# Kernel tuning notes

Hardware: AMD Instinct MI355X
Metric: run time of the kernel (lower is better)

## Reference

```python
import jax, jax.numpy as jnp
import numpy as np

N = 4096      # nodes
HID = 512     # hidden_size
HEADS = 8
DH = HID // HEADS
EPS = 1e-5    # BatchNorm eps


def setup_inputs() -> dict:
    key = jax.random.key(0)
    ks = jax.random.split(key, 16)
    h = jax.random.normal(ks[0], (N, HID), jnp.float32)
    # sparse adjacency (~degree 32) with self-loops so every row has a neighbor
    A = (jax.random.uniform(ks[1], (N, N)) < 0.008).astype(jnp.float32)
    A = jnp.maximum(A, jnp.eye(N, dtype=jnp.float32))
    w = lambda k, shp: jax.random.normal(k, shp, jnp.float32) * 0.02
    return {
        "A": A, "h": h,
        "Wq": w(ks[2], (HID, HID)), "bq": jnp.zeros((HID,), jnp.float32),
        "Wk": w(ks[3], (HID, HID)), "bk": jnp.zeros((HID,), jnp.float32),
        "Wv": w(ks[4], (HID, HID)), "bv": jnp.zeros((HID,), jnp.float32),
        "Wo": w(ks[5], (HID, HID)), "bo": jnp.zeros((HID,), jnp.float32),
        "bn1_g": jnp.ones((HID,), jnp.float32), "bn1_b": jnp.zeros((HID,), jnp.float32),
        "bn2_g": jnp.ones((HID,), jnp.float32), "bn2_b": jnp.zeros((HID,), jnp.float32),
        "W1": w(ks[6], (HID, 2 * HID)), "b1": jnp.zeros((2 * HID,), jnp.float32),
        "W2": w(ks[7], (2 * HID, HID)), "b2": jnp.zeros((HID,), jnp.float32),
    }


def _batchnorm(x, g, b):
    # BatchNorm1d training mode: stats over the node (batch) axis
    m = jnp.mean(x, axis=0)
    v = jnp.var(x, axis=0)
    return g * (x - m) * jax.lax.rsqrt(v + EPS) + b


def _layer(A, h, Wq, bq, Wk, bk, Wv, bv, Wo, bo,
           bn1_g, bn1_b, bn2_g, bn2_b, W1, b1, W2, b2):
    n = h.shape[0]
    q = (h @ Wq + bq).reshape(n, HEADS, DH)
    k = (h @ Wk + bk).reshape(n, HEADS, DH)
    v = (h @ Wv + bv).reshape(n, HEADS, DH)
    # scores [heads, n, m], masked by adjacency
    scores = jnp.einsum('nhd,mhd->hnm', q, k) / np.float32(np.sqrt(DH))
    scores = jnp.where(A[None, :, :] > 0, scores, jnp.float32(-1e9))
    attn = jax.nn.softmax(scores, axis=-1)
    o = jnp.einsum('hnm,mhd->nhd', attn, v).reshape(n, HID)
    h1 = o @ Wo + bo
    h = _batchnorm(h + h1, bn1_g, bn1_b)
    h2 = jax.nn.relu(h @ W1 + b1) @ W2 + b2
    return _batchnorm(h + h2, bn2_g, bn2_b)


def reference(A, h, Wq, bq, Wk, bk, Wv, bv, Wo, bo,
              bn1_g, bn1_b, bn2_g, bn2_b, W1, b1, W2, b2):
    return _layer(A, h, Wq, bq, Wk, bk, Wv, bv, Wo, bo,
                  bn1_g, bn1_b, bn2_g, bn2_b, W1, b1, W2, b2)
```

## Files before the change

kernel.cpp:

```cpp
#include <hip/hip_runtime.h>

#define N_NODES 4096
#define HID 512
#define HEADS 8
#define DH 64
#define EPS 1e-5f
#define MAXD 128

typedef __attribute__((ext_vector_type(8))) short bf16x8;
typedef __attribute__((ext_vector_type(4))) float f32x4;

__device__ __forceinline__ unsigned short f2bf(float f) {
    unsigned int u = __float_as_uint(f);
    unsigned int r = (u + 0x7FFFu + ((u >> 16) & 1u)) >> 16;
    return (unsigned short)r;
}
__device__ __forceinline__ float blo(unsigned int u) {
    return __uint_as_float(u << 16);
}
__device__ __forceinline__ float bhi(unsigned int u) {
    return __uint_as_float(u & 0xffff0000u);
}

__device__ __forceinline__ void gld_lds16(const void* g, void* l) {
    __builtin_amdgcn_global_load_lds(
        (const __attribute__((address_space(1))) unsigned int*)g,
        (__attribute__((address_space(3))) unsigned int*)l, 16, 0, 0);
}

template<int BN, int EPI>
__global__ __launch_bounds__(256) void gemm_bf16(
    const unsigned short* __restrict__ Xb, const unsigned short* __restrict__ Wt,
    const float* __restrict__ bias, const float* __restrict__ res,
    float* __restrict__ outf, unsigned short* __restrict__ outb,
    float* __restrict__ sum, float* __restrict__ sumsq,
    int K, int Nc)
{
    constexpr int WM = (BN == 128) ? 4 : 2;
    __shared__ __align__(16) unsigned short As[128 * 64];
    __shared__ __align__(16) unsigned short Bs[BN * 64];

    const int tid = threadIdx.x;
    const int lane = tid & 63;
    const int wv = tid >> 6;
    const int wm = (BN == 128) ? (wv >> 1) : wv;
    const int wn = (BN == 128) ? (wv & 1) : 0;
    const int m0 = blockIdx.y * 128, n0 = blockIdx.x * BN;
    const int lc = lane & 15, lq = lane >> 4;

    const int srow = tid >> 3;
    const int schunk = (tid & 7) ^ (srow & 7);
    unsigned short* ldsA = As + tid * 8;
    unsigned short* ldsB = Bs + tid * 8;

    const int rs0 = lq ^ (lc & 7);
    const int rs1 = (4 + lq) ^ (lc & 7);

    f32x4 acc[WM][4] = {};

    for (int k0 = 0; k0 < K; k0 += 64) {
        const unsigned short* gA = Xb + (size_t)(m0 + srow) * K + k0 + schunk * 8;
        const unsigned short* gB = Wt + (size_t)(n0 + srow) * K + k0 + schunk * 8;
        #pragma unroll
        for (int p = 0; p < 4; ++p)
            gld_lds16(gA + (size_t)(p * 32) * K, ldsA + p * 2048);
        #pragma unroll
        for (int p = 0; p < BN / 32; ++p)
            gld_lds16(gB + (size_t)(p * 32) * K, ldsB + p * 2048);
        __syncthreads();

        #pragma unroll
        for (int h = 0; h < 2; ++h) {
            const int rs = h ? rs1 : rs0;
            bf16x8 af[WM], bfr[4];
            #pragma unroll
            for (int i = 0; i < WM; ++i)
                af[i] = *(const bf16x8*)&As[(wm * (WM * 16) + i * 16 + lc) * 64 + rs * 8];
            #pragma unroll
            for (int j = 0; j < 4; ++j)
                bfr[j] = *(const bf16x8*)&Bs[(wn * 64 + j * 16 + lc) * 64 + rs * 8];
            #pragma unroll
            for (int i = 0; i < WM; ++i)
                #pragma unroll
                for (int j = 0; j < 4; ++j)
                    acc[i][j] = __builtin_amdgcn_mfma_f32_16x16x32_bf16(af[i], bfr[j], acc[i][j], 0, 0, 0);
        }
        __syncthreads();
    }

    float cs[4] = {}, css[4] = {};
    #pragma unroll
    for (int i = 0; i < WM; ++i) {
        #pragma unroll
        for (int j = 0; j < 4; ++j) {
            const int gr0 = m0 + wm * (WM * 16) + i * 16 + lq * 4;
            const int gc = n0 + wn * 64 + j * 16 + lc;
            const float bi = bias[gc];
            #pragma unroll
            for (int r = 0; r < 4; ++r) {
                float val = acc[i][j][r] + bi;
                size_t off = (size_t)(gr0 + r) * Nc + gc;
                if (EPI == 0)      outb[off] = f2bf(val);
                else if (EPI == 1) outb[off] = f2bf(fmaxf(val, 0.f));
                else {
                    val += res[off];
                    outf[off] = val;
                    cs[j] += val; css[j] += val * val;
                }
            }
        }
    }
    if (EPI == 2) {
        #pragma unroll
        for (int j = 0; j < 4; ++j) {
            float s = cs[j], ss = css[j];
            s += __shfl_xor(s, 16); s += __shfl_xor(s, 32);
            ss += __shfl_xor(ss, 16); ss += __shfl_xor(ss, 32);
            if (lq == 0) {
                const int gc = n0 + wn * 64 + j * 16 + lc;
                atomicAdd(&sum[gc], s);
                atomicAdd(&sumsq[gc], ss);
            }
        }
    }
}

__global__ __launch_bounds__(256) void prep_all(
    const float* __restrict__ Wq, const float* __restrict__ Wk,
    const float* __restrict__ Wv, const float* __restrict__ Wo,
    const float* __restrict__ W1, const float* __restrict__ W2,
    const float* __restrict__ h,
    const float* __restrict__ bq, const float* __restrict__ bk,
    const float* __restrict__ bv,
    unsigned short* __restrict__ wqkvT, unsigned short* __restrict__ woT,
    unsigned short* __restrict__ w1T, unsigned short* __restrict__ w2T,
    unsigned int* __restrict__ hb, float* __restrict__ bqkv,
    float* __restrict__ st)
{
    const int z = blockIdx.z;
    if (z < 6) {
        const float* in; unsigned short* out; int R, C;
        switch (z) {
            case 0: in = Wq; out = wqkvT;          R = 512;  C = 512;  break;
            case 1: in = Wk; out = wqkvT + 262144; R = 512;  C = 512;  break;
            case 2: in = Wv; out = wqkvT + 524288; R = 512;  C = 512;  break;
            case 3: in = Wo; out = woT;            R = 512;  C = 512;  break;
            case 4: in = W1; out = w1T;            R = 512;  C = 1024; break;
            default: in = W2; out = w2T;           R = 1024; C = 512;  break;
        }
        const int bc = blockIdx.x * 32, br = blockIdx.y * 32;
        if (bc >= C || br >= R) return;
        __shared__ float tile[32][33];
        const int tx = threadIdx.x & 31, ty = threadIdx.x >> 5;
        #pragma unroll
        for (int r = ty; r < 32; r += 8)
            tile[r][tx] = in[(size_t)(br + r) * C + bc + tx];
        __syncthreads();
        #pragma unroll
        for (int r = ty; r < 32; r += 8)
            out[(size_t)(bc + r) * R + br + tx] = f2bf(tile[tx][r]);
    } else if (z == 6) {
        const int blk = blockIdx.y * 32 + blockIdx.x;
        const int i = blk * 512 + threadIdx.x * 2;
        const float4* in4 = (const float4*)h;
        #pragma unroll
        for (int u = 0; u < 2; ++u) {
            float4 f = in4[i + u];
            hb[(i + u) * 2]     = (unsigned int)f2bf(f.x) | ((unsigned int)f2bf(f.y) << 16);
            hb[(i + u) * 2 + 1] = (unsigned int)f2bf(f.z) | ((unsigned int)f2bf(f.w) << 16);
        }
    } else {
        const int blk = blockIdx.y * 32 + blockIdx.x;
        const int i = blk * 256 + threadIdx.x;
        if (i < 1536) bqkv[i] = i < 512 ? bq[i] : (i < 1024 ? bk[i - 512] : bv[i - 1024]);
        if (i < 2048) st[i] = 0.0f;
    }
}

__global__ __launch_bounds__(256) void sparse_attn5(
    const float* __restrict__ A, const unsigned short* __restrict__ qkv,
    unsigned short* __restrict__ o)
{
    const int n = blockIdx.x;
    const int tid = threadIdx.x;
    const int wv = tid >> 6, lane = tid & 63;

    __shared__ int s_idx[MAXD];
    __shared__ float s_p[8][MAXD];
    __shared__ int s_cnt[4];

    const float4* r4 = (const float4*)(A + (size_t)n * N_NODES);
    float4 av[4];
    #pragma unroll
    for (int t = 0; t < 4; ++t)
        av[t] = r4[wv * 256 + t * 64 + lane];

    const unsigned long long lt = (1ull << lane) - 1ull;
    int cnt = 0;
    #pragma unroll
    for (int t = 0; t < 4; ++t) {
        #pragma unroll
        for (int b = 0; b < 4; ++b) {
            float vb = (b == 0) ? av[t].x : (b == 1) ? av[t].y : (b == 2) ? av[t].z : av[t].w;
            cnt += __popcll(__ballot(vb > 0.0f));
        }
    }
    if (lane == 0) s_cnt[wv] = cnt;
    __syncthreads();
    int base = 0, total = 0;
    #pragma unroll
    for (int w = 0; w < 4; ++w) {
        if (w < wv) base += s_cnt[w];
        total += s_cnt[w];
    }
    const int d = total < MAXD ? total : MAXD;
    #pragma unroll
    for (int t = 0; t < 4; ++t) {
        #pragma unroll
        for (int b = 0; b < 4; ++b) {
            float vb = (b == 0) ? av[t].x : (b == 1) ? av[t].y : (b == 2) ? av[t].z : av[t].w;
            unsigned long long m = __ballot(vb > 0.0f);
            if (vb > 0.0f) {
                int p = base + __popcll(m & lt);
                if (p < MAXD) s_idx[p] = wv * 1024 + t * 256 + lane * 4 + b;
            }
            base += __popcll(m);
        }
    }
    __syncthreads();

    const int jl = lane >> 3;
    const int dgs = lane & 7;
    const int jl2 = lane >> 4;
    const int dga = lane & 15;
    const int h0 = wv, h1 = wv + 4;

    const unsigned short* qp = qkv + (size_t)n * 1536 + dgs * 8;
    uint4 qa = *(const uint4*)(qp + h0 * 64);
    uint4 qb = *(const uint4*)(qp + h1 * 64);
    const float a0 = blo(qa.x), a1 = bhi(qa.x), a2 = blo(qa.y), a3 = bhi(qa.y);
    const float a4 = blo(qa.z), a5 = bhi(qa.z), a6 = blo(qa.w), a7 = bhi(qa.w);
    const float b0 = blo(qb.x), b1 = bhi(qb.x), b2 = blo(qb.y), b3 = bhi(qb.y);
    const float b4 = blo(qb.z), b5 = bhi(qb.z), b6 = blo(qb.w), b7 = bhi(qb.w);

    uint4 ka = {0, 0, 0, 0}, kb = {0, 0, 0, 0};
    if (jl < d) {
        const unsigned short* p = qkv + (size_t)s_idx[jl] * 1536 + 512 + dgs * 8;
        ka = *(const uint4*)(p + h0 * 64);
        kb = *(const uint4*)(p + h1 * 64);
    }
    for (int j0 = 0; j0 < d; j0 += 8) {
        const uint4 ca = ka, cb = kb;
        const int jn = j0 + 8 + jl;
        if (jn < d) {
            const unsigned short* p = qkv + (size_t)s_idx[jn] * 1536 + 512 + dgs * 8;
            ka = *(const uint4*)(p + h0 * 64);
            kb = *(const uint4*)(p + h1 * 64);
        }
        const int jc = j0 + jl;
        float s0 = 0.f, s1 = 0.f;
        if (jc < d) {
            s0 = a0 * blo(ca.x) + a1 * bhi(ca.x) + a2 * blo(ca.y) + a3 * bhi(ca.y)
               + a4 * blo(ca.z) + a5 * bhi(ca.z) + a6 * blo(ca.w) + a7 * bhi(ca.w);
            s1 = b0 * blo(cb.x) + b1 * bhi(cb.x) + b2 * blo(cb.y) + b3 * bhi(cb.y)
               + b4 * blo(cb.z) + b5 * bhi(cb.z) + b6 * blo(cb.w) + b7 * bhi(cb.w);
        }
        s0 += __shfl_xor(s0, 1); s1 += __shfl_xor(s1, 1);
        s0 += __shfl_xor(s0, 2); s1 += __shfl_xor(s1, 2);
        s0 += __shfl_xor(s0, 4); s1 += __shfl_xor(s1, 4);
        if (dgs == 0 && jc < d) {
            s_p[h0][jc] = s0 * 0.125f;
            s_p[h1][jc] = s1 * 0.125f;
        }
    }

    float inv0, inv1;
    #pragma unroll
    for (int hh = 0; hh < 2; ++hh) {
        float* sp = s_p[hh ? h1 : h0];
        float mx = -1e30f;
        for (int j = lane; j < d; j += 64) mx = fmaxf(mx, sp[j]);
        #pragma unroll
        for (int off = 32; off; off >>= 1) mx = fmaxf(mx, __shfl_xor(mx, off));
        float sum = 0.f;
        for (int j = lane; j < d; j += 64) {
            float e = __expf(sp[j] - mx);
            sp[j] = e;
            sum += e;
        }
        #pragma unroll
        for (int off = 32; off; off >>= 1) sum += __shfl_xor(sum, off);
        if (hh) inv1 = 1.0f / sum; else inv0 = 1.0f / sum;
    }

    float x0 = 0.f, x1 = 0.f, x2 = 0.f, x3 = 0.f;
    float y0 = 0.f, y1 = 0.f, y2 = 0.f, y3 = 0.f;
    uint2 va = {0, 0}, vb = {0, 0};
    if (jl2 < d) {
        const unsigned short* p = qkv + (size_t)s_idx[jl2] * 1536 + 1024 + dga * 4;
        va = *(const uint2*)(p + h0 * 64);
        vb = *(const uint2*)(p + h1 * 64);
    }
    for (int j0 = 0; j0 < d; j0 += 4) {
        const uint2 ca = va, cb = vb;
        const int jn = j0 + 4 + jl2;
        if (jn < d) {
            const unsigned short* p = qkv + (size_t)s_idx[jn] * 1536 + 1024 + dga * 4;
            va = *(const uint2*)(p + h0 * 64);
            vb = *(const uint2*)(p + h1 * 64);
        }
        const int jc = j0 + jl2;
        if (jc < d) {
            const float p0 = s_p[h0][jc], p1 = s_p[h1][jc];
            x0 += p0 * blo(ca.x); x1 += p0 * bhi(ca.x);
            x2 += p0 * blo(ca.y); x3 += p0 * bhi(ca.y);
            y0 += p1 * blo(cb.x); y1 += p1 * bhi(cb.x);
            y2 += p1 * blo(cb.y); y3 += p1 * bhi(cb.y);
        }
    }
    x0 += __shfl_xor(x0, 16); x0 += __shfl_xor(x0, 32);
    x1 += __shfl_xor(x1, 16); x1 += __shfl_xor(x1, 32);
    x2 += __shfl_xor(x2, 16); x2 += __shfl_xor(x2, 32);
    x3 += __shfl_xor(x3, 16); x3 += __shfl_xor(x3, 32);
    y0 += __shfl_xor(y0, 16); y0 += __shfl_xor(y0, 32);
    y1 += __shfl_xor(y1, 16); y1 += __shfl_xor(y1, 32);
    y2 += __shfl_xor(y2, 16); y2 += __shfl_xor(y2, 32);
    y3 += __shfl_xor(y3, 16); y3 += __shfl_xor(y3, 32);
    if (jl2 == 0) {
        uint2 w0, w1;
        w0.x = (unsigned int)f2bf(x0 * inv0) | ((unsigned int)f2bf(x1 * inv0) << 16);
        w0.y = (unsigned int)f2bf(x2 * inv0) | ((unsigned int)f2bf(x3 * inv0) << 16);
        w1.x = (unsigned int)f2bf(y0 * inv1) | ((unsigned int)f2bf(y1 * inv1) << 16);
        w1.y = (unsigned int)f2bf(y2 * inv1) | ((unsigned int)f2bf(y3 * inv1) << 16);
        *(uint2*)(o + (size_t)n * 512 + h0 * 64 + dga * 4) = w0;
        *(uint2*)(o + (size_t)n * 512 + h1 * 64 + dga * 4) = w1;
    }
}

__global__ __launch_bounds__(256) void bn_apply4(
    const float4* __restrict__ x, const float* __restrict__ sum,
    const float* __restrict__ sumsq, const float* __restrict__ g,
    const float* __restrict__ b, float4* __restrict__ yf,
    uint2* __restrict__ yb)
{
    const int i = blockIdx.x * 256 + threadIdx.x;
    const int c4 = i & 127;
    const float4 s4 = ((const float4*)sum)[c4];
    const float4 q4 = ((const float4*)sumsq)[c4];
    const float4 g4 = ((const float4*)g)[c4];
    const float4 b4 = ((const float4*)b)[c4];
    const float4 xv = x[i];
    const float kN = 1.0f / N_NODES;
    float4 r;
    { float m = s4.x * kN; r.x = g4.x * (xv.x - m) * rsqrtf(q4.x * kN - m * m + EPS) + b4.x; }
    { float m = s4.y * kN; r.y = g4.y * (xv.y - m) * rsqrtf(q4.y * kN - m * m + EPS) + b4.y; }
    { float m = s4.z * kN; r.z = g4.z * (xv.z - m) * rsqrtf(q4.z * kN - m * m + EPS) + b4.z; }
    { float m = s4.w * kN; r.w = g4.w * (xv.w - m) * rsqrtf(q4.w * kN - m * m + EPS) + b4.w; }
    yf[i] = r;
    if (yb) {
        uint2 p;
        p.x = (unsigned int)f2bf(r.x) | ((unsigned int)f2bf(r.y) << 16);
        p.y = (unsigned int)f2bf(r.z) | ((unsigned int)f2bf(r.w) << 16);
        yb[i] = p;
    }
}


extern "C" void kernel_launch(void* const* d_in, const int* in_sizes, int n_in,
                              void* d_out, int out_size, void* d_ws, size_t ws_size,
                              hipStream_t stream)
{
    const float* A   = (const float*)d_in[0];
    const float* h   = (const float*)d_in[1];
    const float* Wq  = (const float*)d_in[2];
    const float* bq  = (const float*)d_in[3];
    const float* Wk  = (const float*)d_in[4];
    const float* bk  = (const float*)d_in[5];
    const float* Wv  = (const float*)d_in[6];
    const float* bv  = (const float*)d_in[7];
    const float* Wo  = (const float*)d_in[8];
    const float* bo  = (const float*)d_in[9];
    const float* g1  = (const float*)d_in[10];
    const float* b1g = (const float*)d_in[11];
    const float* g2  = (const float*)d_in[12];
    const float* b2g = (const float*)d_in[13];
    const float* W1  = (const float*)d_in[14];
    const float* b1  = (const float*)d_in[15];
    const float* W2  = (const float*)d_in[16];
    const float* b2  = (const float*)d_in[17];
    float* out = (float*)d_out;

    float* ws = (float*)d_ws;
    unsigned short* hb    = (unsigned short*)(ws);
    unsigned short* qkvb  = (unsigned short*)(ws + 1048576);
    unsigned short* o_bf  = (unsigned short*)(ws + 4194304);
    unsigned short* wqkvT = (unsigned short*)(ws + 5242880);
    unsigned short* woT   = (unsigned short*)(ws + 5636096);
    unsigned short* w1T   = (unsigned short*)(ws + 5767168);
    unsigned short* w2T   = (unsigned short*)(ws + 6029312);
    unsigned short* t_b   = (unsigned short*)(ws + 6291456);
    float* x1   = ws + 8388608;
    float* x2   = ws + 10485760;
    unsigned short* xb1_b = (unsigned short*)(ws + 12582912);
    float* bqkv = ws + 13631488;
    float* st   = ws + 13633024;

    prep_all<<<dim3(32, 32, 8), dim3(256), 0, stream>>>(
        Wq, Wk, Wv, Wo, W1, W2, h, bq, bk, bv,
        wqkvT, woT, w1T, w2T, (unsigned int*)hb, bqkv, st);

    gemm_bf16<128, 0><<<dim3(12, 32), dim3(256), 0, stream>>>(
        hb, wqkvT, bqkv, nullptr, nullptr, qkvb, nullptr, nullptr, 512, 1536);

    sparse_attn5<<<dim3(N_NODES), dim3(256), 0, stream>>>(A, qkvb, o_bf);

    gemm_bf16<64, 2><<<dim3(8, 32), dim3(256), 0, stream>>>(
        o_bf, woT, bo, h, x1, nullptr, st, st + 512, 512, 512);

    bn_apply4<<<dim3(2048), dim3(256), 0, stream>>>(
        (const float4*)x1, st, st + 512, g1, b1g, (float4*)x1, (uint2*)xb1_b);

    gemm_bf16<128, 1><<<dim3(8, 32), dim3(256), 0, stream>>>(
        xb1_b, w1T, b1, nullptr, nullptr, t_b, nullptr, nullptr, 512, 1024);
    gemm_bf16<64, 2><<<dim3(8, 32), dim3(256), 0, stream>>>(
        t_b, w2T, b2, x1, x2, nullptr, st + 1024, st + 1536, 1024, 512);

    bn_apply4<<<dim3(2048), dim3(256), 0, stream>>>(
        (const float4*)x2, st + 1024, st + 1536, g2, b2g, (float4*)out, nullptr);

    (void)in_sizes; (void)n_in; (void)out_size; (void)ws_size;
}
```

Before: 242.5 us.

## Retile GEMMs to 64-wide N tiles and read bf16 residual for FFN

Result: faster. 232.9 us (-4.0%).

```diff
diff --git a/kernel.cpp b/kernel.cpp
--- a/kernel.cpp
+++ b/kernel.cpp
@@ -28,31 +28,30 @@
         (__attribute__((address_space(3))) unsigned int*)l, 16, 0, 0);
 }
 
-template<int BN, int EPI>
+template<int TM, int EPI>
 __global__ __launch_bounds__(256) void gemm_bf16(
     const unsigned short* __restrict__ Xb, const unsigned short* __restrict__ Wt,
     const float* __restrict__ bias, const float* __restrict__ res,
+    const unsigned short* __restrict__ resb,
     float* __restrict__ outf, unsigned short* __restrict__ outb,
     float* __restrict__ sum, float* __restrict__ sumsq,
     int K, int Nc)
 {
-    constexpr int WM = (BN == 128) ? 4 : 2;
-    __shared__ __align__(16) unsigned short As[128 * 64];
-    __shared__ __align__(16) unsigned short Bs[BN * 64];
+    constexpr int WM = TM / 64;
+    __shared__ __align__(16) unsigned short As[TM * 64];
+    __shared__ __align__(16) unsigned short Bs[64 * 64];
 
     const int tid = threadIdx.x;
     const int lane = tid & 63;
     const int wv = tid >> 6;
-    const int wm = (BN == 128) ? (wv >> 1) : wv;
-    const int wn = (BN == 128) ? (wv & 1) : 0;
-    const int m0 = blockIdx.y * 128, n0 = blockIdx.x * BN;
+    const int m0 = blockIdx.y * TM, n0 = blockIdx.x * 64;
     const int lc = lane & 15, lq = lane >> 4;
+    const int rowbase = wv * (WM * 16);
 
     const int srow = tid >> 3;
     const int schunk = (tid & 7) ^ (srow & 7);
     unsigned short* ldsA = As + tid * 8;
     unsigned short* ldsB = Bs + tid * 8;
-
     const int rs0 = lq ^ (lc & 7);
     const int rs1 = (4 + lq) ^ (lc & 7);
 
@@ -62,23 +61,23 @@
         const unsigned short* gA = Xb + (size_t)(m0 + srow) * K + k0 + schunk * 8;
         const unsigned short* gB = Wt + (size_t)(n0 + srow) * K + k0 + schunk * 8;
         #pragma unroll
-        for (int p = 0; p < 4; ++p)
+        for (int p = 0; p < TM / 32; ++p)
             gld_lds16(gA + (size_t)(p * 32) * K, ldsA + p * 2048);
         #pragma unroll
-        for (int p = 0; p < BN / 32; ++p)
+        for (int p = 0; p < 2; ++p)
             gld_lds16(gB + (size_t)(p * 32) * K, ldsB + p * 2048);
         __syncthreads();
 
         #pragma unroll
-        for (int h = 0; h < 2; ++h) {
-            const int rs = h ? rs1 : rs0;
+        for (int hh = 0; hh < 2; ++hh) {
+            const int rs = hh ? rs1 : rs0;
             bf16x8 af[WM], bfr[4];
             #pragma unroll
             for (int i = 0; i < WM; ++i)
-                af[i] = *(const bf16x8*)&As[(wm * (WM * 16) + i * 16 + lc) * 64 + rs * 8];
+                af[i] = *(const bf16x8*)&As[(rowbase + i * 16 + lc) * 64 + rs * 8];
             #pragma unroll
             for (int j = 0; j < 4; ++j)
-                bfr[j] = *(const bf16x8*)&Bs[(wn * 64 + j * 16 + lc) * 64 + rs * 8];
+                bfr[j] = *(const bf16x8*)&Bs[(j * 16 + lc) * 64 + rs * 8];
             #pragma unroll
             for (int i = 0; i < WM; ++i)
                 #pragma unroll
@@ -93,8 +92,8 @@
     for (int i = 0; i < WM; ++i) {
         #pragma unroll
         for (int j = 0; j < 4; ++j) {
-            const int gr0 = m0 + wm * (WM * 16) + i * 16 + lq * 4;
-            const int gc = n0 + wn * 64 + j * 16 + lc;
+            const int gr0 = m0 + rowbase + i * 16 + lq * 4;
+            const int gc = n0 + j * 16 + lc;
             const float bi = bias[gc];
             #pragma unroll
             for (int r = 0; r < 4; ++r) {
@@ -103,21 +102,22 @@
                 if (EPI == 0)      outb[off] = f2bf(val);
                 else if (EPI == 1) outb[off] = f2bf(fmaxf(val, 0.f));
                 else {
-                    val += res[off];
+                    if (EPI == 2) val += res[off];
+                    else          val += blo((unsigned int)resb[off]);
                     outf[off] = val;
                     cs[j] += val; css[j] += val * val;
                 }
             }
         }
     }
-    if (EPI == 2) {
+    if (EPI >= 2) {
         #pragma unroll
         for (int j = 0; j < 4; ++j) {
             float s = cs[j], ss = css[j];
             s += __shfl_xor(s, 16); s += __shfl_xor(s, 32);
             ss += __shfl_xor(ss, 16); ss += __shfl_xor(ss, 32);
             if (lq == 0) {
-                const int gc = n0 + wn * 64 + j * 16 + lc;
+                const int gc = n0 + j * 16 + lc;
                 atomicAdd(&sum[gc], s);
                 atomicAdd(&sumsq[gc], ss);
             }
@@ -356,7 +356,7 @@
     { float m = s4.y * kN; r.y = g4.y * (xv.y - m) * rsqrtf(q4.y * kN - m * m + EPS) + b4.y; }
     { float m = s4.z * kN; r.z = g4.z * (xv.z - m) * rsqrtf(q4.z * kN - m * m + EPS) + b4.z; }
     { float m = s4.w * kN; r.w = g4.w * (xv.w - m) * rsqrtf(q4.w * kN - m * m + EPS) + b4.w; }
-    yf[i] = r;
+    if (yf) yf[i] = r;
     if (yb) {
         uint2 p;
         p.x = (unsigned int)f2bf(r.x) | ((unsigned int)f2bf(r.y) << 16);
@@ -409,21 +409,22 @@
         Wq, Wk, Wv, Wo, W1, W2, h, bq, bk, bv,
         wqkvT, woT, w1T, w2T, (unsigned int*)hb, bqkv, st);
 
-    gemm_bf16<128, 0><<<dim3(12, 32), dim3(256), 0, stream>>>(
-        hb, wqkvT, bqkv, nullptr, nullptr, qkvb, nullptr, nullptr, 512, 1536);
+    gemm_bf16<128, 0><<<dim3(24, 32), dim3(256), 0, stream>>>(
+        hb, wqkvT, bqkv, nullptr, nullptr, nullptr, qkvb, nullptr, nullptr, 512, 1536);
 
     sparse_attn5<<<dim3(N_NODES), dim3(256), 0, stream>>>(A, qkvb, o_bf);
 
-    gemm_bf16<64, 2><<<dim3(8, 32), dim3(256), 0, stream>>>(
-        o_bf, woT, bo, h, x1, nullptr, st, st + 512, 512, 512);
+    gemm_bf16<64, 2><<<dim3(8, 64), dim3(256), 0, stream>>>(
+        o_bf, woT, bo, h, nullptr, x1, nullptr, st, st + 512, 512, 512);
 
     bn_apply4<<<dim3(2048), dim3(256), 0, stream>>>(
-        (const float4*)x1, st, st + 512, g1, b1g, (float4*)x1, (uint2*)xb1_b);
-
-    gemm_bf16<128, 1><<<dim3(8, 32), dim3(256), 0, stream>>>(
-        xb1_b, w1T, b1, nullptr, nullptr, t_b, nullptr, nullptr, 512, 1024);
-    gemm_bf16<64, 2><<<dim3(8, 32), dim3(256), 0, stream>>>(
-        t_b, w2T, b2, x1, x2, nullptr, st + 1024, st + 1536, 1024, 512);
+        (const float4*)x1, st, st + 512, g1, b1g, nullptr, (uint2*)xb1_b);
+
+    gemm_bf16<128, 1><<<dim3(16, 32), dim3(256), 0, stream>>>(
+        xb1_b, w1T, b1, nullptr, nullptr, nullptr, t_b, nullptr, nullptr, 512, 1024);
+
+    gemm_bf16<64, 3><<<dim3(8, 64), dim3(256), 0, stream>>>(
+        t_b, w2T, b2, nullptr, xb1_b, x2, nullptr, st + 1024, st + 1536, 1024, 512);
 
     bn_apply4<<<dim3(2048), dim3(256), 0, stream>>>(
         (const float4*)x2, st + 1024, st + 1536, g2, b2g, (float4*)out, nullptr);
```
